# Kernel optimization log

Hardware: AMD Instinct MI355X
Metric: run time of the kernel (lower is better)

The kernel has to match this reference:

```python
import jax, jax.numpy as jnp
import numpy as np

N_NODES = 100000
N_EDGES = 3200000
IN_DIM = 8
HID = 64
N_LAYERS = 3
LN_EPS = 1e-5


def setup_inputs() -> dict:
    key = jax.random.key(0)
    ks = jax.random.split(key, 10)
    x = jax.random.normal(ks[0], (N_NODES, IN_DIM), dtype=jnp.float32)
    edge_src = jax.random.randint(ks[1], (N_EDGES,), 0, N_NODES, dtype=jnp.int32)
    edge_dst = jax.random.randint(ks[2], (N_EDGES,), 0, N_NODES, dtype=jnp.int32)
    # parameters
    W_in = jax.random.normal(ks[3], (HID, IN_DIM), dtype=jnp.float32) * 0.1
    b_in = jnp.zeros((HID,), dtype=jnp.float32)
    Ws_self = jax.random.normal(ks[4], (N_LAYERS, HID, HID), dtype=jnp.float32) * 0.1
    Ws_neigh = jax.random.normal(ks[5], (N_LAYERS, HID, HID), dtype=jnp.float32) * 0.1
    biases = jnp.zeros((N_LAYERS, HID), dtype=jnp.float32)
    gammas = jnp.ones((N_LAYERS, HID), dtype=jnp.float32)
    betas = jnp.zeros((N_LAYERS, HID), dtype=jnp.float32)
    return {"x": x, "edge_src": edge_src, "edge_dst": edge_dst,
            "W_in": W_in, "b_in": b_in, "Ws_self": Ws_self,
            "Ws_neigh": Ws_neigh, "biases": biases,
            "gammas": gammas, "betas": betas}


def _layer_norm(h, gamma, beta):
    mu = jnp.mean(h, axis=-1, keepdims=True)
    var = jnp.mean((h - mu) ** 2, axis=-1, keepdims=True)
    return (h - mu) * jax.lax.rsqrt(var + LN_EPS) * gamma + beta


def reference(x, edge_src, edge_dst, W_in, b_in, Ws_self, Ws_neigh, biases, gammas, betas):
    n = x.shape[0]
    # deg[v] = number of neighbors gathered for node v (edges ending at v)
    deg = jax.ops.segment_sum(jnp.ones_like(edge_dst, dtype=jnp.float32), edge_dst,
                              num_segments=n)  # (n,)
    inv_deg = jnp.where(deg > 0, 1.0 / jnp.maximum(deg, 1.0), 0.0)[:, None]

    h = jax.nn.relu(x @ W_in.T + b_in)  # (n, HID); dropout is identity in eval
    for l in range(N_LAYERS):
        # mean neighbor features: gather + scatter-add + normalize
        neigh_sum = jax.ops.segment_sum(h[edge_src], edge_dst, num_segments=n)
        neigh_mean = neigh_sum * inv_deg  # zero rows where deg==0, as in original
        h_self = h @ Ws_self[l].T
        h_neigh = neigh_mean @ Ws_neigh[l].T  # linear has no bias -> 0 when deg==0
        h_l = _layer_norm(h_self + h_neigh + biases[l], gammas[l], betas[l])
        h = h + jax.nn.relu(h_l)  # residual from DrBCEncoder
    return h
```

## Files before the change

### kernel.cpp

```cpp
#include <hip/hip_runtime.h>

#define HID 64
#define BSHIFT 9
#define NPB 512
#define P3TILE 4096
#define HISTB 512
#define PREPB 96

typedef unsigned int uint;
typedef unsigned short ushort;
typedef unsigned char uchar;
typedef float f32x2 __attribute__((ext_vector_type(2)));
typedef float f32x4 __attribute__((ext_vector_type(4)));
typedef short bf16x8 __attribute__((ext_vector_type(8)));

__device__ inline ushort f2b(float f) {
    uint u = __float_as_uint(f);
    return (ushort)((u + 0x7fffu + ((u >> 16) & 1u)) >> 16);
}

__device__ inline float b2f(ushort b) { return __uint_as_float((uint)b << 16); }

__device__ inline void accf8(f32x2* a, uint4 hv) {
    a[0] += __builtin_bit_cast(f32x2, __builtin_amdgcn_cvt_pk_f32_fp8(hv.x, false));
    a[1] += __builtin_bit_cast(f32x2, __builtin_amdgcn_cvt_pk_f32_fp8(hv.x, true));
    a[2] += __builtin_bit_cast(f32x2, __builtin_amdgcn_cvt_pk_f32_fp8(hv.y, false));
    a[3] += __builtin_bit_cast(f32x2, __builtin_amdgcn_cvt_pk_f32_fp8(hv.y, true));
    a[4] += __builtin_bit_cast(f32x2, __builtin_amdgcn_cvt_pk_f32_fp8(hv.z, false));
    a[5] += __builtin_bit_cast(f32x2, __builtin_amdgcn_cvt_pk_f32_fp8(hv.z, true));
    a[6] += __builtin_bit_cast(f32x2, __builtin_amdgcn_cvt_pk_f32_fp8(hv.w, false));
    a[7] += __builtin_bit_cast(f32x2, __builtin_amdgcn_cvt_pk_f32_fp8(hv.w, true));
}

__device__ inline uchar f2fp8(float f) {
    return (uchar)(__builtin_amdgcn_cvt_pk_fp8_f32(f, f, 0, false) & 0xff);
}


__global__ __launch_bounds__(256) void hist_input(const int* __restrict__ dst,
                                                  int* __restrict__ bcnt, int e, int nb,
                                                  const float* __restrict__ x,
                                                  const float* __restrict__ W_in,
                                                  const float* __restrict__ b_in,
                                                  ushort* __restrict__ hb,
                                                  uchar* __restrict__ h8, int n,
                                                  int inb,
                                                  const float* __restrict__ Ws,
                                                  const float* __restrict__ Wn,
                                                  ushort* __restrict__ Wcat) {
    __shared__ float smem[576];
    int t = threadIdx.x;
    int b = blockIdx.x;
    if (b < HISTB) {
        int* lh = (int*)smem;
        lh[t] = 0;
        __syncthreads();
        for (int i = b * 256 + t; i < e; i += HISTB * 256)
            atomicAdd(&lh[dst[i] >> BSHIFT], 1);
        __syncthreads();
        if (t < nb && lh[t]) atomicAdd(&bcnt[t], lh[t]);
        return;
    }
    if (b >= HISTB + inb) {
        int i = (b - HISTB - inb) * 256 + t;
        if (i < 3 * 8192) {
            int l = i >> 13;
            int r = i & 8191;
            int j = r >> 7;
            int k = r & 127;
            float v = (k < 64) ? Ws[l * 4096 + j * 64 + k]
                               : Wn[l * 4096 + j * 64 + (k - 64)];
            Wcat[i] = f2b(v);
        }
        return;
    }
    int ib = b - HISTB;
    float* WlT = smem;
    float* bl = smem + 512;
    for (int i = t; i < 512; i += 256) {
        int j = i >> 3, k = i & 7;
        WlT[k * 64 + j] = W_in[i];
    }
    if (t < 64) bl[t] = b_in[t];
    __syncthreads();
    int total2 = n * 32;
    for (int i = ib * 256 + t; i < total2; i += inb * 256) {
        int v = i >> 5;
        int jp = i & 31;
        int j0 = jp * 2, j1 = jp * 2 + 1;
        const float* xr = x + (size_t)v * 8;
        float s0 = bl[j0], s1 = bl[j1];
#pragma unroll
        for (int k = 0; k < 8; ++k) {
            float xv = xr[k];
            s0 += xv * WlT[k * 64 + j0];
            s1 += xv * WlT[k * 64 + j1];
        }
        float o0 = fmaxf(s0, 0.0f), o1 = fmaxf(s1, 0.0f);
        ((uint*)hb)[i] = (uint)f2b(o0) | ((uint)f2b(o1) << 16);
        int pk = __builtin_amdgcn_cvt_pk_fp8_f32(o0, o1, 0, false);
        *(ushort*)&h8[(size_t)2 * i] = (ushort)(pk & 0xffff);
    }
}

__global__ void bucket_scan(const int* __restrict__ bcnt, int* __restrict__ bbase,
                            int* __restrict__ bcur, int* __restrict__ offsets,
                            int e, int nb, int n) {
    __shared__ int sd[256];
    int t = threadIdx.x;
    int v = (t < nb) ? bcnt[t] : 0;
    sd[t] = v;
    __syncthreads();
    for (int off = 1; off < 256; off <<= 1) {
        int u = (t >= off) ? sd[t - off] : 0;
        __syncthreads();
        sd[t] += u;
        __syncthreads();
    }
    int excl = t ? sd[t - 1] : 0;
    if (t < nb) { bbase[t] = excl; bcur[t] = excl; }
    if (t == nb) bbase[t] = e;
    if (t == 0) offsets[n] = e;
}

__global__ __launch_bounds__(256) void partition(const int* __restrict__ src,
                                                 const int* __restrict__ dst,
                                                 int* __restrict__ bcur,
                                                 int* __restrict__ pair, int e, int nb) {
    __shared__ int lh[256], cb[256];
    int t = threadIdx.x;
    int base = blockIdx.x * P3TILE;
    lh[t] = 0;
    __syncthreads();
    int s[16], d[16], r[16];
    if (base + P3TILE <= e) {
        const int4* s4 = (const int4*)(src + base);
        const int4* d4 = (const int4*)(dst + base);
#pragma unroll
        for (int k = 0; k < 4; ++k) {
            int4 sv = s4[t * 4 + k];
            int4 dv = d4[t * 4 + k];
            s[k * 4 + 0] = sv.x; s[k * 4 + 1] = sv.y;
            s[k * 4 + 2] = sv.z; s[k * 4 + 3] = sv.w;
            d[k * 4 + 0] = dv.x; d[k * 4 + 1] = dv.y;
            d[k * 4 + 2] = dv.z; d[k * 4 + 3] = dv.w;
        }
#pragma unroll
        for (int k = 0; k < 16; ++k)
            r[k] = atomicAdd(&lh[d[k] >> BSHIFT], 1);
        __syncthreads();
        if (t < nb && lh[t]) cb[t] = atomicAdd(&bcur[t], lh[t]);
        __syncthreads();
#pragma unroll
        for (int k = 0; k < 16; ++k)
            pair[cb[d[k] >> BSHIFT] + r[k]] = (s[k] << BSHIFT) | (d[k] & (NPB - 1));
    } else {
#pragma unroll
        for (int k = 0; k < 16; ++k) {
            int i = base + t * 16 + k;
            if (i < e) {
                s[k] = src[i];
                d[k] = dst[i];
                r[k] = atomicAdd(&lh[d[k] >> BSHIFT], 1);
            }
        }
        __syncthreads();
        if (t < nb && lh[t]) cb[t] = atomicAdd(&bcur[t], lh[t]);
        __syncthreads();
#pragma unroll
        for (int k = 0; k < 16; ++k) {
            int i = base + t * 16 + k;
            if (i < e)
                pair[cb[d[k] >> BSHIFT] + r[k]] = (s[k] << BSHIFT) | (d[k] & (NPB - 1));
        }
    }
}

__global__ __launch_bounds__(1024) void build_csr(const int* __restrict__ pair,
                                                  const int* __restrict__ bbase,
                                                  int* __restrict__ offsets,
                                                  float* __restrict__ invdeg,
                                                  int* __restrict__ col, int n) {
    __shared__ int bins[NPB], cur[NPB], sd[NPB];
    int b = blockIdx.x, t = threadIdx.x;
    int cbase = bbase[b], cend = bbase[b + 1];
    int v0 = b << BSHIFT;
    if (t < NPB) bins[t] = 0;
    __syncthreads();
    for (int i = cbase + t; i < cend; i += 1024)
        atomicAdd(&bins[pair[i] & (NPB - 1)], 1);
    __syncthreads();
    int d = (t < NPB) ? bins[t] : 0;
    if (t < NPB) sd[t] = d;
    __syncthreads();
    for (int off = 1; off < NPB; off <<= 1) {
        int u = (t < NPB && t >= off) ? sd[t - off] : 0;
        __syncthreads();
        if (t < NPB) sd[t] += u;
        __syncthreads();
    }
    if (t < NPB) {
        int excl = sd[t] - d;
        cur[t] = excl;
        int v = v0 + t;
        if (v < n) {
            offsets[v] = cbase + excl;
            invdeg[v] = d > 0 ? 1.0f / (float)d : 0.0f;
        }
    }
    __syncthreads();
    for (int i = cbase + t; i < cend; i += 1024) {
        int p = pair[i];
        int pos = atomicAdd(&cur[p & (NPB - 1)], 1);
        col[cbase + pos] = p >> BSHIFT;
    }
}


__global__ __launch_bounds__(256) void aggregate_fp8(const uchar* __restrict__ h8,
                                                     ushort* __restrict__ nmb,
                                                     const int* __restrict__ offsets,
                                                     const int* __restrict__ col,
                                                     const float* __restrict__ invdeg,
                                                     int n) {
    int t = threadIdx.x, lane = t & 63, wid = t >> 6;
    int q = lane >> 4;
    int fl = lane & 15;
    int e4 = lane & 3;
    int sl = (lane >> 2) & 3;
    int nwaves = gridDim.x * 4;
    int ngrp = (n + 3) >> 2;
    for (int w = blockIdx.x * 4 + wid; w < ngrp; w += nwaves) {
        int v = w * 4 + q;
        bool valid = v < n;
        int vv = valid ? v : n - 1;
        int o0 = offsets[vv], o1 = offsets[vv + 1];
        int deg = o1 - o0;
        const int* cp = col + o0;
        int deg16 = deg & ~15;
        f32x2 acc2[8];
        float* af = (float*)acc2;
#pragma unroll
        for (int k = 0; k < 8; ++k) acc2[k] = f32x2{0.f, 0.f};
        for (int base = 0; base < deg16; base += 16) {
            int idx16 = cp[base + fl];
#pragma unroll
            for (int jj = 0; jj < 16; jj += 4) {
                int ne = __shfl(idx16, q * 16 + jj + sl);
                uint4 hv = *(const uint4*)&h8[(size_t)ne * HID + e4 * 16];
                accf8(acc2, hv);
            }
        }
        for (int jj = 0; jj < 16; jj += 4) {
            if (deg16 + jj >= deg) break;
            int j = deg16 + jj + sl;
            if (j < deg) {
                int ne = cp[j];
                uint4 hv = *(const uint4*)&h8[(size_t)ne * HID + e4 * 16];
                accf8(acc2, hv);
            }
        }
#pragma unroll
        for (int k = 0; k < 16; ++k) {
            af[k] += __shfl_xor(af[k], 4);
            af[k] += __shfl_xor(af[k], 8);
        }
        if (valid && sl == 0) {
            float s = invdeg[vv];
            uint4 lo, hi;
            lo.x = (uint)f2b(af[0] * s) | ((uint)f2b(af[1] * s) << 16);
            lo.y = (uint)f2b(af[2] * s) | ((uint)f2b(af[3] * s) << 16);
            lo.z = (uint)f2b(af[4] * s) | ((uint)f2b(af[5] * s) << 16);
            lo.w = (uint)f2b(af[6] * s) | ((uint)f2b(af[7] * s) << 16);
            hi.x = (uint)f2b(af[8] * s) | ((uint)f2b(af[9] * s) << 16);
            hi.y = (uint)f2b(af[10] * s) | ((uint)f2b(af[11] * s) << 16);
            hi.z = (uint)f2b(af[12] * s) | ((uint)f2b(af[13] * s) << 16);
            hi.w = (uint)f2b(af[14] * s) | ((uint)f2b(af[15] * s) << 16);
            *(uint4*)&nmb[(size_t)v * HID + e4 * 16] = lo;
            *(uint4*)&nmb[(size_t)v * HID + e4 * 16 + 8] = hi;
        }
    }
}


__global__ __launch_bounds__(256) void transform_mfma(
    const ushort* __restrict__ hbm, const ushort* __restrict__ nmb,
    ushort* __restrict__ hbout, uchar* __restrict__ h8out,
    float* __restrict__ outF, const ushort* __restrict__ Wcat,
    const float* __restrict__ bias, const float* __restrict__ gamma,
    const float* __restrict__ beta, int n, int last) {
    int t = threadIdx.x, lane = t & 63, wid = t >> 6;
    int c = lane & 15, g = lane >> 4;
    bf16x8 Bf[4][4];
#pragma unroll
    for (int tt = 0; tt < 4; ++tt)
#pragma unroll
        for (int s = 0; s < 4; ++s)
            Bf[s][tt] = *(const bf16x8*)&Wcat[(tt * 16 + c) * 128 + s * 32 + g * 8];
    float bcol[4], gcol[4], btc[4];
#pragma unroll
    for (int tt = 0; tt < 4; ++tt) {
        bcol[tt] = bias[tt * 16 + c];
        gcol[tt] = gamma[tt * 16 + c];
        btc[tt] = beta[tt * 16 + c];
    }
    int ntiles = (n + 15) >> 4;
    int nw = gridDim.x * 4;
    for (int tile = blockIdx.x * 4 + wid; tile < ntiles; tile += nw) {
        int m0 = tile << 4;
        int node = m0 + c;
        int nodeL = node < n ? node : n - 1;
        bf16x8 Af[4];
#pragma unroll
        for (int s = 0; s < 2; ++s)
            Af[s] = *(const bf16x8*)&hbm[(size_t)nodeL * HID + s * 32 + g * 8];
#pragma unroll
        for (int s = 0; s < 2; ++s)
            Af[2 + s] = *(const bf16x8*)&nmb[(size_t)nodeL * HID + s * 32 + g * 8];
        f32x4 acc[4] = {{0, 0, 0, 0}, {0, 0, 0, 0}, {0, 0, 0, 0}, {0, 0, 0, 0}};
#pragma unroll
        for (int tt = 0; tt < 4; ++tt)
#pragma unroll
            for (int s = 0; s < 4; ++s)
                acc[tt] = __builtin_amdgcn_mfma_f32_16x16x32_bf16(Af[s], Bf[s][tt],
                                                                 acc[tt], 0, 0, 0);
        float v[4][4];
#pragma unroll
        for (int tt = 0; tt < 4; ++tt)
#pragma unroll
            for (int r = 0; r < 4; ++r) v[tt][r] = acc[tt][r] + bcol[tt];
#pragma unroll
        for (int r = 0; r < 4; ++r) {
            float s = v[0][r] + v[1][r] + v[2][r] + v[3][r];
            s += __shfl_xor(s, 1);
            s += __shfl_xor(s, 2);
            s += __shfl_xor(s, 4);
            s += __shfl_xor(s, 8);
            float mu = s * (1.0f / 64.0f);
            float ss = 0.f;
#pragma unroll
            for (int tt = 0; tt < 4; ++tt) {
                float d = v[tt][r] - mu;
                ss += d * d;
            }
            ss += __shfl_xor(ss, 1);
            ss += __shfl_xor(ss, 2);
            ss += __shfl_xor(ss, 4);
            ss += __shfl_xor(ss, 8);
            float inv = rsqrtf(ss * (1.0f / 64.0f) + 1e-5f);
            int nr = m0 + g * 4 + r;
            if (nr < n) {
#pragma unroll
                for (int tt = 0; tt < 4; ++tt) {
                    int j = tt * 16 + c;
                    float hl = (v[tt][r] - mu) * inv * gcol[tt] + btc[tt];
                    float hv = b2f(hbm[(size_t)nr * HID + j]);
                    float o = hv + fmaxf(hl, 0.0f);
                    if (last) {
                        outF[(size_t)nr * HID + j] = o;
                    } else {
                        hbout[(size_t)nr * HID + j] = f2b(o);
                        h8out[(size_t)nr * HID + j] = f2fp8(o);
                    }
                }
            }
        }
    }
}


extern "C" void kernel_launch(void* const* d_in, const int* in_sizes, int n_in,
                              void* d_out, int out_size, void* d_ws, size_t ws_size,
                              hipStream_t stream) {
    const float* x = (const float*)d_in[0];
    const int* edge_src = (const int*)d_in[1];
    const int* edge_dst = (const int*)d_in[2];
    const float* W_in = (const float*)d_in[3];
    const float* b_in = (const float*)d_in[4];
    const float* Ws_self = (const float*)d_in[5];
    const float* Ws_neigh = (const float*)d_in[6];
    const float* biases = (const float*)d_in[7];
    const float* gammas = (const float*)d_in[8];
    const float* betas = (const float*)d_in[9];
    float* out = (float*)d_out;

    int n = in_sizes[0] / 8;
    int e = in_sizes[1];
    int nb = (n + NPB - 1) >> BSHIFT;

    char* w = (char*)d_ws;
    size_t off = 0;
    auto carve = [&](size_t bytes) -> void* {
        void* p = w + off;
        off = (off + bytes + 255) & ~(size_t)255;
        return p;
    };
    int* offsets = (int*)carve((size_t)(n + 1) * 4);
    float* invdeg = (float*)carve((size_t)n * 4);
    int* bcnt = (int*)carve(1024 * 4);
    int* bbase = (int*)carve(1024 * 4);
    int* bcur = (int*)carve(1024 * 4);
    int* col = (int*)carve((size_t)e * 4);
    int* pairbuf = (int*)carve((size_t)e * 4);
    ushort* hb = (ushort*)carve((size_t)n * HID * 2);
    ushort* nm16 = (ushort*)carve((size_t)n * HID * 2);
    uchar* h8 = (uchar*)carve((size_t)n * HID);
    ushort* Wcat = (ushort*)carve(3 * 64 * 128 * 2);
    (void)ws_size;

    hipMemsetAsync(bcnt, 0, 1024 * 4, stream);
    hist_input<<<HISTB + 2048 + PREPB, 256, 0, stream>>>(edge_dst, bcnt, e, nb,
                                                         x, W_in, b_in, hb, h8, n,
                                                         2048, Ws_self, Ws_neigh, Wcat);
    bucket_scan<<<1, 256, 0, stream>>>(bcnt, bbase, bcur, offsets, e, nb, n);
    partition<<<(e + P3TILE - 1) / P3TILE, 256, 0, stream>>>(edge_src, edge_dst, bcur,
                                                            pairbuf, e, nb);
    build_csr<<<nb, 1024, 0, stream>>>(pairbuf, bbase, offsets, invdeg, col, n);

    int tfblocks = ((n + 15) / 16 + 3) / 4;
    for (int l = 0; l < 3; ++l) {
        aggregate_fp8<<<2048, 256, 0, stream>>>(h8, nm16, offsets, col, invdeg, n);
        transform_mfma<<<tfblocks, 256, 0, stream>>>(hb, nm16, hb, h8, out,
                                                     Wcat + (size_t)l * 8192,
                                                     biases + l * 64, gammas + l * 64,
                                                     betas + l * 64, n, l == 2 ? 1 : 0);
    }
}
```

Baseline: 303.7 us.

## Split fp8 feature table into two 32-byte halves aggregated in separate passes

Stores the fp8 node features as two separate 32-column tables, one 3.2 MB each, instead of one 64-byte-row table. The neighbour aggregation becomes two launches, each gathering one half, so each pass's random-access working set is smaller and more likely to stay cache-resident. The cost is reading the CSR edge list twice per layer, an extra kernel launch, and a 32-byte gather granularity that may use memory transactions less efficiently.

```diff
diff --git a/kernel.cpp b/kernel.cpp
--- a/kernel.cpp
+++ b/kernel.cpp
@@ -43,7 +43,8 @@
                                                   const float* __restrict__ W_in,
                                                   const float* __restrict__ b_in,
                                                   ushort* __restrict__ hb,
-                                                  uchar* __restrict__ h8, int n,
+                                                  uchar* __restrict__ h8a,
+                                                  uchar* __restrict__ h8b, int n,
                                                   int inb,
                                                   const float* __restrict__ Ws,
                                                   const float* __restrict__ Wn,
@@ -99,7 +100,8 @@
         float o0 = fmaxf(s0, 0.0f), o1 = fmaxf(s1, 0.0f);
         ((uint*)hb)[i] = (uint)f2b(o0) | ((uint)f2b(o1) << 16);
         int pk = __builtin_amdgcn_cvt_pk_fp8_f32(o0, o1, 0, false);
-        *(ushort*)&h8[(size_t)2 * i] = (ushort)(pk & 0xffff);
+        uchar* hp = (jp < 16) ? h8a : h8b;
+        *(ushort*)&hp[(size_t)v * 32 + (size_t)(jp & 15) * 2] = (ushort)(pk & 0xffff);
     }
 }
 
@@ -217,17 +219,18 @@
 }
 
 
-__global__ __launch_bounds__(256) void aggregate_fp8(const uchar* __restrict__ h8,
-                                                     ushort* __restrict__ nmb,
-                                                     const int* __restrict__ offsets,
-                                                     const int* __restrict__ col,
-                                                     const float* __restrict__ invdeg,
-                                                     int n) {
+template <int PHASE>
+__global__ __launch_bounds__(256) void aggregate_half(const uchar* __restrict__ tab,
+                                                      ushort* __restrict__ nmb,
+                                                      const int* __restrict__ offsets,
+                                                      const int* __restrict__ col,
+                                                      const float* __restrict__ invdeg,
+                                                      int n) {
     int t = threadIdx.x, lane = t & 63, wid = t >> 6;
     int q = lane >> 4;
     int fl = lane & 15;
-    int e4 = lane & 3;
-    int sl = (lane >> 2) & 3;
+    int e2 = lane & 1;
+    int sl = (lane >> 1) & 7;
     int nwaves = gridDim.x * 4;
     int ngrp = (n + 3) >> 2;
     for (int w = blockIdx.x * 4 + wid; w < ngrp; w += nwaves) {
@@ -245,23 +248,24 @@
         for (int base = 0; base < deg16; base += 16) {
             int idx16 = cp[base + fl];
 #pragma unroll
-            for (int jj = 0; jj < 16; jj += 4) {
+            for (int jj = 0; jj < 16; jj += 8) {
                 int ne = __shfl(idx16, q * 16 + jj + sl);
-                uint4 hv = *(const uint4*)&h8[(size_t)ne * HID + e4 * 16];
+                uint4 hv = *(const uint4*)&tab[(size_t)ne * 32 + e2 * 16];
                 accf8(acc2, hv);
             }
         }
-        for (int jj = 0; jj < 16; jj += 4) {
+        for (int jj = 0; jj < 16; jj += 8) {
             if (deg16 + jj >= deg) break;
             int j = deg16 + jj + sl;
             if (j < deg) {
                 int ne = cp[j];
-                uint4 hv = *(const uint4*)&h8[(size_t)ne * HID + e4 * 16];
+                uint4 hv = *(const uint4*)&tab[(size_t)ne * 32 + e2 * 16];
                 accf8(acc2, hv);
             }
         }
 #pragma unroll
         for (int k = 0; k < 16; ++k) {
+            af[k] += __shfl_xor(af[k], 2);
             af[k] += __shfl_xor(af[k], 4);
             af[k] += __shfl_xor(af[k], 8);
         }
@@ -276,8 +280,9 @@
             hi.y = (uint)f2b(af[10] * s) | ((uint)f2b(af[11] * s) << 16);
             hi.z = (uint)f2b(af[12] * s) | ((uint)f2b(af[13] * s) << 16);
             hi.w = (uint)f2b(af[14] * s) | ((uint)f2b(af[15] * s) << 16);
-            *(uint4*)&nmb[(size_t)v * HID + e4 * 16] = lo;
-            *(uint4*)&nmb[(size_t)v * HID + e4 * 16 + 8] = hi;
+            ushort* dst = nmb + (size_t)v * HID + PHASE * 32 + e2 * 16;
+            *(uint4*)dst = lo;
+            *(uint4*)(dst + 8) = hi;
         }
     }
 }
@@ -285,7 +290,8 @@
 
 __global__ __launch_bounds__(256) void transform_mfma(
     const ushort* __restrict__ hbm, const ushort* __restrict__ nmb,
-    ushort* __restrict__ hbout, uchar* __restrict__ h8out,
+    ushort* __restrict__ hbout, uchar* __restrict__ h8a,
+    uchar* __restrict__ h8b,
     float* __restrict__ outF, const ushort* __restrict__ Wcat,
     const float* __restrict__ bias, const float* __restrict__ gamma,
     const float* __restrict__ beta, int n, int last) {
@@ -360,7 +366,8 @@
                         outF[(size_t)nr * HID + j] = o;
                     } else {
                         hbout[(size_t)nr * HID + j] = f2b(o);
-                        h8out[(size_t)nr * HID + j] = f2fp8(o);
+                        uchar* hp = (tt < 2) ? h8a : h8b;
+                        hp[(size_t)nr * 32 + (tt & 1) * 16 + c] = f2fp8(o);
                     }
                 }
             }
@@ -404,13 +411,14 @@
     int* pairbuf = (int*)carve((size_t)e * 4);
     ushort* hb = (ushort*)carve((size_t)n * HID * 2);
     ushort* nm16 = (ushort*)carve((size_t)n * HID * 2);
-    uchar* h8 = (uchar*)carve((size_t)n * HID);
+    uchar* h8a = (uchar*)carve((size_t)n * 32);
+    uchar* h8b = (uchar*)carve((size_t)n * 32);
     ushort* Wcat = (ushort*)carve(3 * 64 * 128 * 2);
     (void)ws_size;
 
     hipMemsetAsync(bcnt, 0, 1024 * 4, stream);
     hist_input<<<HISTB + 2048 + PREPB, 256, 0, stream>>>(edge_dst, bcnt, e, nb,
-                                                         x, W_in, b_in, hb, h8, n,
+                                                         x, W_in, b_in, hb, h8a, h8b, n,
                                                          2048, Ws_self, Ws_neigh, Wcat);
     bucket_scan<<<1, 256, 0, stream>>>(bcnt, bbase, bcur, offsets, e, nb, n);
     partition<<<(e + P3TILE - 1) / P3TILE, 256, 0, stream>>>(edge_src, edge_dst, bcur,
@@ -419,8 +427,9 @@
 
     int tfblocks = ((n + 15) / 16 + 3) / 4;
     for (int l = 0; l < 3; ++l) {
-        aggregate_fp8<<<2048, 256, 0, stream>>>(h8, nm16, offsets, col, invdeg, n);
-        transform_mfma<<<tfblocks, 256, 0, stream>>>(hb, nm16, hb, h8, out,
+        aggregate_half<0><<<2048, 256, 0, stream>>>(h8a, nm16, offsets, col, invdeg, n);
+        aggregate_half<1><<<2048, 256, 0, stream>>>(h8b, nm16, offsets, col, invdeg, n);
+        transform_mfma<<<tfblocks, 256, 0, stream>>>(hb, nm16, hb, h8a, h8b, out,
                                                      Wcat + (size_t)l * 8192,
                                                      biases + l * 64, gammas + l * 64,
                                                      betas + l * 64, n, l == 2 ? 1 : 0);
```

Measured after the change: 363.2 us. +19.6%, slower.

## Fuse neighbor aggregation and MFMA transform into one per-tile kernel

Applied to the files above, without the earlier changes.

Merges the FP8 gather-aggregate kernel and the MFMA linear+layernorm+residual kernel into a single kernel. Each wave aggregates its own 16-node tile, keeps the neighbor means in LDS and feeds them directly to the MFMA. This removes the bf16 neighbor-mean round trip through global memory and one launch per layer, and it ping-pongs the fp8 feature buffers to avoid read/write races. In exchange, the aggregation loses its grid-stride load balancing, and the register pressure of both phases is combined in one kernel, which may lower occupancy.

```diff
diff --git a/kernel.cpp b/kernel.cpp
--- a/kernel.cpp
+++ b/kernel.cpp
@@ -217,23 +217,28 @@
 }
 
 
-__global__ __launch_bounds__(256) void aggregate_fp8(const uchar* __restrict__ h8,
-                                                     ushort* __restrict__ nmb,
-                                                     const int* __restrict__ offsets,
-                                                     const int* __restrict__ col,
-                                                     const float* __restrict__ invdeg,
-                                                     int n) {
+template <int LAST>
+__global__ __launch_bounds__(256) void agg_tf(
+    const uchar* __restrict__ h8in, const ushort* __restrict__ hbm,
+    ushort* __restrict__ hbout, uchar* __restrict__ h8out,
+    float* __restrict__ outF,
+    const int* __restrict__ offsets, const int* __restrict__ col,
+    const float* __restrict__ invdeg,
+    const ushort* __restrict__ Wcat, const float* __restrict__ bias,
+    const float* __restrict__ gamma, const float* __restrict__ beta, int n) {
+    __shared__ ushort nmlds[4][16][72];
     int t = threadIdx.x, lane = t & 63, wid = t >> 6;
+    int ntiles = (n + 15) >> 4;
+    int tile = blockIdx.x * 4 + wid;
+    if (tile >= ntiles) return;
+    int m0 = tile << 4;
     int q = lane >> 4;
     int fl = lane & 15;
     int e4 = lane & 3;
     int sl = (lane >> 2) & 3;
-    int nwaves = gridDim.x * 4;
-    int ngrp = (n + 3) >> 2;
-    for (int w = blockIdx.x * 4 + wid; w < ngrp; w += nwaves) {
-        int v = w * 4 + q;
-        bool valid = v < n;
-        int vv = valid ? v : n - 1;
+    for (int p = 0; p < 4; ++p) {
+        int v = m0 + p * 4 + q;
+        int vv = v < n ? v : n - 1;
         int o0 = offsets[vv], o1 = offsets[vv + 1];
         int deg = o1 - o0;
         const int* cp = col + o0;
@@ -247,7 +252,7 @@
 #pragma unroll
             for (int jj = 0; jj < 16; jj += 4) {
                 int ne = __shfl(idx16, q * 16 + jj + sl);
-                uint4 hv = *(const uint4*)&h8[(size_t)ne * HID + e4 * 16];
+                uint4 hv = *(const uint4*)&h8in[(size_t)ne * HID + e4 * 16];
                 accf8(acc2, hv);
             }
         }
@@ -256,7 +261,7 @@
             int j = deg16 + jj + sl;
             if (j < deg) {
                 int ne = cp[j];
-                uint4 hv = *(const uint4*)&h8[(size_t)ne * HID + e4 * 16];
+                uint4 hv = *(const uint4*)&h8in[(size_t)ne * HID + e4 * 16];
                 accf8(acc2, hv);
             }
         }
@@ -265,7 +270,7 @@
             af[k] += __shfl_xor(af[k], 4);
             af[k] += __shfl_xor(af[k], 8);
         }
-        if (valid && sl == 0) {
+        if (sl == 0) {
             float s = invdeg[vv];
             uint4 lo, hi;
             lo.x = (uint)f2b(af[0] * s) | ((uint)f2b(af[1] * s) << 16);
@@ -276,20 +281,10 @@
             hi.y = (uint)f2b(af[10] * s) | ((uint)f2b(af[11] * s) << 16);
             hi.z = (uint)f2b(af[12] * s) | ((uint)f2b(af[13] * s) << 16);
             hi.w = (uint)f2b(af[14] * s) | ((uint)f2b(af[15] * s) << 16);
-            *(uint4*)&nmb[(size_t)v * HID + e4 * 16] = lo;
-            *(uint4*)&nmb[(size_t)v * HID + e4 * 16 + 8] = hi;
-        }
-    }
-}
-
-
-__global__ __launch_bounds__(256) void transform_mfma(
-    const ushort* __restrict__ hbm, const ushort* __restrict__ nmb,
-    ushort* __restrict__ hbout, uchar* __restrict__ h8out,
-    float* __restrict__ outF, const ushort* __restrict__ Wcat,
-    const float* __restrict__ bias, const float* __restrict__ gamma,
-    const float* __restrict__ beta, int n, int last) {
-    int t = threadIdx.x, lane = t & 63, wid = t >> 6;
+            *(uint4*)&nmlds[wid][p * 4 + q][e4 * 16] = lo;
+            *(uint4*)&nmlds[wid][p * 4 + q][e4 * 16 + 8] = hi;
+        }
+    }
     int c = lane & 15, g = lane >> 4;
     bf16x8 Bf[4][4];
 #pragma unroll
@@ -304,64 +299,59 @@
         gcol[tt] = gamma[tt * 16 + c];
         btc[tt] = beta[tt * 16 + c];
     }
-    int ntiles = (n + 15) >> 4;
-    int nw = gridDim.x * 4;
-    for (int tile = blockIdx.x * 4 + wid; tile < ntiles; tile += nw) {
-        int m0 = tile << 4;
-        int node = m0 + c;
-        int nodeL = node < n ? node : n - 1;
-        bf16x8 Af[4];
-#pragma unroll
-        for (int s = 0; s < 2; ++s)
-            Af[s] = *(const bf16x8*)&hbm[(size_t)nodeL * HID + s * 32 + g * 8];
-#pragma unroll
-        for (int s = 0; s < 2; ++s)
-            Af[2 + s] = *(const bf16x8*)&nmb[(size_t)nodeL * HID + s * 32 + g * 8];
-        f32x4 acc[4] = {{0, 0, 0, 0}, {0, 0, 0, 0}, {0, 0, 0, 0}, {0, 0, 0, 0}};
-#pragma unroll
-        for (int tt = 0; tt < 4; ++tt)
-#pragma unroll
-            for (int s = 0; s < 4; ++s)
-                acc[tt] = __builtin_amdgcn_mfma_f32_16x16x32_bf16(Af[s], Bf[s][tt],
-                                                                 acc[tt], 0, 0, 0);
-        float v[4][4];
-#pragma unroll
-        for (int tt = 0; tt < 4; ++tt)
-#pragma unroll
-            for (int r = 0; r < 4; ++r) v[tt][r] = acc[tt][r] + bcol[tt];
-#pragma unroll
-        for (int r = 0; r < 4; ++r) {
-            float s = v[0][r] + v[1][r] + v[2][r] + v[3][r];
-            s += __shfl_xor(s, 1);
-            s += __shfl_xor(s, 2);
-            s += __shfl_xor(s, 4);
-            s += __shfl_xor(s, 8);
-            float mu = s * (1.0f / 64.0f);
-            float ss = 0.f;
+    int node = m0 + c;
+    int nodeL = node < n ? node : n - 1;
+    bf16x8 Af[4];
+#pragma unroll
+    for (int s = 0; s < 2; ++s)
+        Af[s] = *(const bf16x8*)&hbm[(size_t)nodeL * HID + s * 32 + g * 8];
+#pragma unroll
+    for (int s = 0; s < 2; ++s)
+        Af[2 + s] = *(const bf16x8*)&nmlds[wid][c][s * 32 + g * 8];
+    f32x4 acc[4] = {{0, 0, 0, 0}, {0, 0, 0, 0}, {0, 0, 0, 0}, {0, 0, 0, 0}};
+#pragma unroll
+    for (int tt = 0; tt < 4; ++tt)
+#pragma unroll
+        for (int s = 0; s < 4; ++s)
+            acc[tt] = __builtin_amdgcn_mfma_f32_16x16x32_bf16(Af[s], Bf[s][tt],
+                                                             acc[tt], 0, 0, 0);
+    float v[4][4];
+#pragma unroll
+    for (int tt = 0; tt < 4; ++tt)
+#pragma unroll
+        for (int r = 0; r < 4; ++r) v[tt][r] = acc[tt][r] + bcol[tt];
+#pragma unroll
+    for (int r = 0; r < 4; ++r) {
+        float s = v[0][r] + v[1][r] + v[2][r] + v[3][r];
+        s += __shfl_xor(s, 1);
+        s += __shfl_xor(s, 2);
+        s += __shfl_xor(s, 4);
+        s += __shfl_xor(s, 8);
+        float mu = s * (1.0f / 64.0f);
+        float ss = 0.f;
+#pragma unroll
+        for (int tt = 0; tt < 4; ++tt) {
+            float d = v[tt][r] - mu;
+            ss += d * d;
+        }
+        ss += __shfl_xor(ss, 1);
+        ss += __shfl_xor(ss, 2);
+        ss += __shfl_xor(ss, 4);
+        ss += __shfl_xor(ss, 8);
+        float inv = rsqrtf(ss * (1.0f / 64.0f) + 1e-5f);
+        int nr = m0 + g * 4 + r;
+        if (nr < n) {
 #pragma unroll
             for (int tt = 0; tt < 4; ++tt) {
-                float d = v[tt][r] - mu;
-                ss += d * d;
-            }
-            ss += __shfl_xor(ss, 1);
-            ss += __shfl_xor(ss, 2);
-            ss += __shfl_xor(ss, 4);
-            ss += __shfl_xor(ss, 8);
-            float inv = rsqrtf(ss * (1.0f / 64.0f) + 1e-5f);
-            int nr = m0 + g * 4 + r;
-            if (nr < n) {
-#pragma unroll
-                for (int tt = 0; tt < 4; ++tt) {
-                    int j = tt * 16 + c;
-                    float hl = (v[tt][r] - mu) * inv * gcol[tt] + btc[tt];
-                    float hv = b2f(hbm[(size_t)nr * HID + j]);
-                    float o = hv + fmaxf(hl, 0.0f);
-                    if (last) {
-                        outF[(size_t)nr * HID + j] = o;
-                    } else {
-                        hbout[(size_t)nr * HID + j] = f2b(o);
-                        h8out[(size_t)nr * HID + j] = f2fp8(o);
-                    }
+                int j = tt * 16 + c;
+                float hl = (v[tt][r] - mu) * inv * gcol[tt] + btc[tt];
+                float hv = b2f(hbm[(size_t)nr * HID + j]);
+                float o = hv + fmaxf(hl, 0.0f);
+                if (LAST) {
+                    outF[(size_t)nr * HID + j] = o;
+                } else {
+                    hbout[(size_t)nr * HID + j] = f2b(o);
+                    h8out[(size_t)nr * HID + j] = f2fp8(o);
                 }
             }
         }
@@ -403,26 +393,38 @@
     int* col = (int*)carve((size_t)e * 4);
     int* pairbuf = (int*)carve((size_t)e * 4);
     ushort* hb = (ushort*)carve((size_t)n * HID * 2);
-    ushort* nm16 = (ushort*)carve((size_t)n * HID * 2);
-    uchar* h8 = (uchar*)carve((size_t)n * HID);
+    uchar* h8A = (uchar*)carve((size_t)n * HID);
+    uchar* h8B = (uchar*)carve((size_t)n * HID);
     ushort* Wcat = (ushort*)carve(3 * 64 * 128 * 2);
     (void)ws_size;
 
     hipMemsetAsync(bcnt, 0, 1024 * 4, stream);
     hist_input<<<HISTB + 2048 + PREPB, 256, 0, stream>>>(edge_dst, bcnt, e, nb,
-                                                         x, W_in, b_in, hb, h8, n,
+                                                         x, W_in, b_in, hb, h8A, n,
                                                          2048, Ws_self, Ws_neigh, Wcat);
     bucket_scan<<<1, 256, 0, stream>>>(bcnt, bbase, bcur, offsets, e, nb, n);
     partition<<<(e + P3TILE - 1) / P3TILE, 256, 0, stream>>>(edge_src, edge_dst, bcur,
                                                             pairbuf, e, nb);
     build_csr<<<nb, 1024, 0, stream>>>(pairbuf, bbase, offsets, invdeg, col, n);
 
-    int tfblocks = ((n + 15) / 16 + 3) / 4;
+    int ntiles = (n + 15) >> 4;
+    int ablocks = (ntiles + 3) / 4;
+    uchar* hin = h8A;
+    uchar* hout = h8B;
     for (int l = 0; l < 3; ++l) {
-        aggregate_fp8<<<2048, 256, 0, stream>>>(h8, nm16, offsets, col, invdeg, n);
-        transform_mfma<<<tfblocks, 256, 0, stream>>>(hb, nm16, hb, h8, out,
-                                                     Wcat + (size_t)l * 8192,
-                                                     biases + l * 64, gammas + l * 64,
-                                                     betas + l * 64, n, l == 2 ? 1 : 0);
-    }
-}
+        if (l < 2) {
+            agg_tf<0><<<ablocks, 256, 0, stream>>>(hin, hb, hb, hout, out,
+                                                   offsets, col, invdeg,
+                                                   Wcat + (size_t)l * 8192,
+                                                   biases + l * 64, gammas + l * 64,
+                                                   betas + l * 64, n);
+        } else {
+            agg_tf<1><<<ablocks, 256, 0, stream>>>(hin, hb, hb, hout, out,
+                                                   offsets, col, invdeg,
+                                                   Wcat + (size_t)l * 8192,
+                                                   biases + l * 64, gammas + l * 64,
+                                                   betas + l * 64, n);
+        }
+        uchar* tmp = hin; hin = hout; hout = tmp;
+    }
+}
```

New measurement: 289.0 us. -4.9%, faster.
